# Optimization experiments

Measured on AMD Instinct MI355X. Metric: run time of the kernel, lower is better.

Reference implementation:

```python
import jax, jax.numpy as jnp
import numpy as np

B, S, HID = 2, 2048, 4096
NH, NKV, HD = 32, 8, 128
MAX_POS = 4096
SCALE = HD ** -0.5


def _rope_tables():
    inv_freq = 1.0 / (10000.0 ** (np.arange(0, HD, 2, dtype=np.float32) / HD))
    t = np.arange(MAX_POS, dtype=np.float32)
    freqs = np.outer(t, inv_freq)              # [MAX_POS, HD/2]
    emb = np.concatenate([freqs, freqs], axis=-1)  # [MAX_POS, HD]
    return jnp.asarray(np.cos(emb)), jnp.asarray(np.sin(emb))


def setup_inputs() -> dict:
    key = jax.random.key(0)
    ks = jax.random.split(key, 6)
    hidden_states = jax.random.normal(ks[0], (B, S, HID), dtype=jnp.float32)
    position_ids = jnp.broadcast_to(jnp.arange(S, dtype=jnp.int64 if jax.config.jax_enable_x64 else jnp.int32), (B, S))
    cos_table, sin_table = _rope_tables()
    # weights stored [in, out] for x @ W
    sd = HID ** -0.5
    Wq = jax.random.normal(ks[1], (HID, NH * HD), dtype=jnp.float32) * sd
    Wk = jax.random.normal(ks[2], (HID, NKV * HD), dtype=jnp.float32) * sd
    Wv = jax.random.normal(ks[3], (HID, NKV * HD), dtype=jnp.float32) * sd
    Wo = jax.random.normal(ks[4], (NH * HD, HID), dtype=jnp.float32) * sd
    return {"hidden_states": hidden_states, "position_ids": position_ids,
            "cos_table": cos_table, "sin_table": sin_table,
            "Wq": Wq, "Wk": Wk, "Wv": Wv, "Wo": Wo}


def _rotate_half(x):
    x1, x2 = jnp.split(x, 2, axis=-1)
    return jnp.concatenate([-x2, x1], axis=-1)


def reference(hidden_states, position_ids, cos_table, sin_table, Wq, Wk, Wv, Wo):
    b, s, _ = hidden_states.shape
    q = (hidden_states @ Wq).reshape(b, s, NH, HD)
    k = (hidden_states @ Wk).reshape(b, s, NKV, HD)
    v = (hidden_states @ Wv).reshape(b, s, NKV, HD)

    # RoPE, cos/sin gathered by position and unsqueezed at head dim (dim=2, bsnd)
    cos = cos_table[position_ids][:, :, None, :]  # [b, s, 1, hd]
    sin = sin_table[position_ids][:, :, None, :]
    q = q * cos + _rotate_half(q) * sin
    k = k * cos + _rotate_half(k) * sin

    # GQA: expand kv heads to match query heads
    rep = NH // NKV
    k = jnp.repeat(k, rep, axis=2)  # [b, s, NH, hd]
    v = jnp.repeat(v, rep, axis=2)

    scores = jnp.einsum('bqnd,bknd->bnqk', q, k) * SCALE  # [b, NH, s, s]
    causal = jnp.tril(jnp.ones((s, s), dtype=bool))
    scores = jnp.where(causal, scores, jnp.finfo(scores.dtype).min)
    probs = jax.nn.softmax(scores, axis=-1)
    attn = jnp.einsum('bnqk,bknd->bqnd', probs, v)  # [b, s, NH, hd]
    attn = attn.reshape(b, s, NH * HD)
    return attn @ Wo
```

## Files before the change

### kernel.cpp

```cpp
#include <hip/hip_runtime.h>
#include <stdint.h>

typedef unsigned short u16;
typedef __bf16 bf16x8 __attribute__((ext_vector_type(8)));
typedef unsigned short u16x8 __attribute__((ext_vector_type(8)));
typedef unsigned short u16x4 __attribute__((ext_vector_type(4)));
typedef float f32x4 __attribute__((ext_vector_type(4)));

#define B_ 2
#define S_ 2048
#define HID_ 4096
#define NH_ 32
#define NKV_ 8
#define HD_ 128
#define NTOT_ 6144
#define SCALE_ 0.08838834764831845f

#define GLD16(gp, lp)                                                     \
  __builtin_amdgcn_global_load_lds(                                       \
      (__attribute__((address_space(1))) void*)(gp),                      \
      (__attribute__((address_space(3))) void*)(lp), 16, 0, 0)

__device__ __forceinline__ u16 f2b(float f) {
  union { float f; uint32_t u; } v; v.f = f;
  uint32_t u = v.u;
  u = u + 0x7fffu + ((u >> 16) & 1u);
  return (u16)(u >> 16);
}
__device__ __forceinline__ float b2f(u16 s) {
  union { uint32_t u; float f; } v; v.u = ((uint32_t)s) << 16;
  return v.f;
}
__device__ __forceinline__ bf16x8 ldb8(const u16* p) {
  u16x8 u = *(const u16x8*)p;
  return __builtin_bit_cast(bf16x8, u);
}
__device__ __forceinline__ bf16x8 ldb8b(const char* p) {
  u16x8 u = *(const u16x8*)p;
  return __builtin_bit_cast(bf16x8, u);
}

__global__ __launch_bounds__(256) void k_convx(const float* __restrict__ src,
                                               u16* __restrict__ dst, int n4) {
  int i = blockIdx.x * 256 + threadIdx.x;
  if (i >= n4) return;
  const float4 v = ((const float4*)src)[i];
  u16x4 o = { f2b(v.x), f2b(v.y), f2b(v.z), f2b(v.w) };
  *(u16x4*)(dst + (size_t)i * 4) = o;
}

__global__ __launch_bounds__(256) void k_convT(const float* __restrict__ src,
                                               u16* __restrict__ dst, int N, int Kd) {
  __shared__ u16 tile[64][65];
  int k0 = blockIdx.x * 64, n0 = blockIdx.y * 64;
  int t = threadIdx.x;
  int rr = t >> 4;
  int cc = (t & 15) * 4;
#pragma unroll
  for (int p = 0; p < 4; ++p) {
    int r = p * 16 + rr;
    float4 v = *(const float4*)&src[(size_t)(k0 + r) * N + n0 + cc];
    tile[cc + 0][r] = f2b(v.x);
    tile[cc + 1][r] = f2b(v.y);
    tile[cc + 2][r] = f2b(v.z);
    tile[cc + 3][r] = f2b(v.w);
  }
  __syncthreads();
#pragma unroll
  for (int p = 0; p < 4; ++p) {
    int n = p * 16 + rr;
    u16x4 o = { tile[n][cc], tile[n][cc + 1], tile[n][cc + 2], tile[n][cc + 3] };
    *(u16x4*)&dst[(size_t)(n0 + n) * Kd + k0 + cc] = o;
  }
}

template <int MODE>
__device__ __forceinline__ void gemm_body(const u16* __restrict__ A,
                                          const u16* __restrict__ Bt,
                                          float* __restrict__ Cf,
                                          u16* __restrict__ Qb,
                                          u16* __restrict__ Kb,
                                          u16* __restrict__ Vb,
                                          int M, int N, int Kd) {
  __shared__ __align__(16) char smem[131072];
  const int NT = Kd >> 6;

  int nwg = gridDim.x * gridDim.y;
  int orig = blockIdx.y * gridDim.x + blockIdx.x;
  int cpx = nwg >> 3;
  int swz = (orig & 7) * cpx + (orig >> 3);
  int bx = swz % gridDim.x, by = swz / gridDim.x;
  int m0 = by * 256, n0 = bx * 256;

  int t = threadIdx.x, lane = t & 63, wave = t >> 6;
  int wr = wave >> 2, wc = wave & 3;
  int lg = lane >> 4, l16 = lane & 15;
  int loff = l16 * 64 + ((lg ^ ((l16 >> 1) & 3)) << 4);
  int srow = lane >> 2, schk = (lane & 3) ^ ((lane >> 3) & 3);

  const u16* Asrc = A  + (size_t)(m0 + wave * 32 + srow) * Kd + schk * 8;
  const u16* Bsrc = Bt + (size_t)(n0 + wave * 32 + srow) * Kd + schk * 8;

  f32x4 acc[8][4] = {};

#define STG_A(kt, kc) do {                                                          \
    char* d_ = smem + (((kt) & 1) << 16) + ((kc) << 14) + (wave << 11);             \
    const u16* s_ = Asrc + (size_t)(kt) * 64 + (kc) * 32;                           \
    GLD16(s_, d_); GLD16(s_ + (size_t)16 * Kd, d_ + 1024); } while (0)
#define STG_B(kt, kc) do {                                                          \
    char* d_ = smem + (((kt) & 1) << 16) + 32768 + ((kc) << 14) + (wave << 11);     \
    const u16* s_ = Bsrc + (size_t)(kt) * 64 + (kc) * 32;                           \
    GLD16(s_, d_); GLD16(s_ + (size_t)16 * Kd, d_ + 1024); } while (0)

  STG_A(0, 0); STG_B(0, 0); STG_A(0, 1); STG_B(0, 1);
  asm volatile("s_waitcnt vmcnt(0)" ::: "memory");
  __syncthreads();

  for (int kt = 0; kt < NT; ++kt) {
    const char* bufA = smem + ((kt & 1) << 16);
    const char* bufB = bufA + 32768;
    bool pf = (kt + 1 < NT);
    bf16x8 bfr[4], af[4];

#pragma unroll
    for (int j = 0; j < 4; ++j) bfr[j] = ldb8b(bufB + ((wc * 4 + j) << 10) + loff);
#pragma unroll
    for (int i = 0; i < 4; ++i) af[i] = ldb8b(bufA + ((wr * 8 + i) << 10) + loff);
    if (pf) STG_A(kt + 1, 0);
    __builtin_amdgcn_s_barrier();
    __builtin_amdgcn_s_setprio(1);
#pragma unroll
    for (int i = 0; i < 4; ++i)
#pragma unroll
      for (int j = 0; j < 4; ++j)
        acc[i][j] = __builtin_amdgcn_mfma_f32_16x16x32_bf16(af[i], bfr[j], acc[i][j], 0, 0, 0);
    __builtin_amdgcn_s_setprio(0);
    __builtin_amdgcn_s_barrier();

#pragma unroll
    for (int i = 0; i < 4; ++i) af[i] = ldb8b(bufA + ((wr * 8 + 4 + i) << 10) + loff);
    if (pf) STG_B(kt + 1, 0);
    __builtin_amdgcn_s_barrier();
    __builtin_amdgcn_s_setprio(1);
#pragma unroll
    for (int i = 0; i < 4; ++i)
#pragma unroll
      for (int j = 0; j < 4; ++j)
        acc[4 + i][j] = __builtin_amdgcn_mfma_f32_16x16x32_bf16(af[i], bfr[j], acc[4 + i][j], 0, 0, 0);
    __builtin_amdgcn_s_setprio(0);
    asm volatile("s_waitcnt vmcnt(4)" ::: "memory");
    __builtin_amdgcn_s_barrier();

#pragma unroll
    for (int j = 0; j < 4; ++j) bfr[j] = ldb8b(bufB + 16384 + ((wc * 4 + j) << 10) + loff);
#pragma unroll
    for (int i = 0; i < 4; ++i) af[i] = ldb8b(bufA + 16384 + ((wr * 8 + i) << 10) + loff);
    if (pf) STG_A(kt + 1, 1);
    __builtin_amdgcn_s_barrier();
    __builtin_amdgcn_s_setprio(1);
#pragma unroll
    for (int i = 0; i < 4; ++i)
#pragma unroll
      for (int j = 0; j < 4; ++j)
        acc[i][j] = __builtin_amdgcn_mfma_f32_16x16x32_bf16(af[i], bfr[j], acc[i][j], 0, 0, 0);
    __builtin_amdgcn_s_setprio(0);
    __builtin_amdgcn_s_barrier();

#pragma unroll
    for (int i = 0; i < 4; ++i) af[i] = ldb8b(bufA + 16384 + ((wr * 8 + 4 + i) << 10) + loff);
    if (pf) STG_B(kt + 1, 1);
    __builtin_amdgcn_s_barrier();
    __builtin_amdgcn_s_setprio(1);
#pragma unroll
    for (int i = 0; i < 4; ++i)
#pragma unroll
      for (int j = 0; j < 4; ++j)
        acc[4 + i][j] = __builtin_amdgcn_mfma_f32_16x16x32_bf16(af[i], bfr[j], acc[4 + i][j], 0, 0, 0);
    __builtin_amdgcn_s_setprio(0);
    asm volatile("s_waitcnt vmcnt(4)" ::: "memory");
    __builtin_amdgcn_s_barrier();
  }
#undef STG_A
#undef STG_B

  if (MODE == 1) {
#pragma unroll
    for (int i = 0; i < 8; ++i)
#pragma unroll
      for (int j = 0; j < 4; ++j)
#pragma unroll
        for (int r = 0; r < 4; ++r) {
          int m = m0 + wr * 128 + i * 16 + lg * 4 + r;
          int n = n0 + wc * 64 + j * 16 + l16;
          Cf[(size_t)m * N + n] = acc[i][j][r];
        }
  } else {
    int slice = (n0 >> 7) + (wc >> 1);
#pragma unroll
    for (int i = 0; i < 8; ++i)
#pragma unroll
      for (int j = 0; j < 4; ++j)
#pragma unroll
        for (int r = 0; r < 4; ++r) {
          int m = m0 + wr * 128 + i * 16 + lg * 4 + r;
          int d = ((wc & 1) << 6) + j * 16 + l16;
          int b = m >> 11, s = m & (S_ - 1);
          u16 val = f2b(acc[i][j][r]);
          if (slice < NH_) {
            Qb[(((size_t)b * NH_ + slice) * S_ + s) * HD_ + d] = val;
          } else if (slice < NH_ + NKV_) {
            Kb[(((size_t)b * NKV_ + (slice - NH_)) * S_ + s) * HD_ + d] = val;
          } else {
            Vb[(((size_t)b * NKV_ + (slice - NH_ - NKV_)) * HD_ + d) * S_ + s] = val;
          }
        }
  }
}

__global__ __launch_bounds__(512, 2) void k_gemm_qkv(const u16* __restrict__ A,
                                                     const u16* __restrict__ Bt,
                                                     u16* __restrict__ Qb,
                                                     u16* __restrict__ Kb,
                                                     u16* __restrict__ Vb,
                                                     int M, int N, int Kd) {
  gemm_body<0>(A, Bt, nullptr, Qb, Kb, Vb, M, N, Kd);
}

__global__ __launch_bounds__(512, 2) void k_gemm_out(const u16* __restrict__ A,
                                                     const u16* __restrict__ Bt,
                                                     float* __restrict__ Cf,
                                                     int M, int N, int Kd) {
  gemm_body<1>(A, Bt, Cf, nullptr, nullptr, nullptr, M, N, Kd);
}

__global__ __launch_bounds__(256) void k_rope(u16* __restrict__ buf, const int* __restrict__ pos,
                                              const float* __restrict__ ct, const float* __restrict__ st,
                                              int H, int rows) {
  int wave = threadIdx.x >> 6, lane = threadIdx.x & 63;
  int row = blockIdx.x * 4 + wave;
  if (row >= rows) return;
  int s = row & (S_ - 1);
  int b = row / (H * S_);
  int p = pos[b * S_ + s];
  size_t base = (size_t)row * HD_;
  float x1 = b2f(buf[base + lane]);
  float x2 = b2f(buf[base + 64 + lane]);
  float c  = ct[(size_t)p * HD_ + lane];
  float sn = st[(size_t)p * HD_ + lane];
  buf[base + lane]      = f2b(x1 * c - x2 * sn);
  buf[base + 64 + lane] = f2b(x2 * c + x1 * sn);
}

__global__ __launch_bounds__(256, 4) void k_attn(const u16* __restrict__ Q,
                                                 const u16* __restrict__ K,
                                                 const u16* __restrict__ Vt,
                                                 u16* __restrict__ Ob) {
  __shared__ __align__(16) char smem[40960];
  const int VS_OFF = 16384, PS_OFF = 32768;

  int bid = blockIdx.x;
  int pid = bid & 15;
  int h   = (bid >> 4) & 31;
  int b   = bid >> 9;
  int kvh = h >> 2;
  int tid = threadIdx.x;
  int wave = tid >> 6, lane = tid & 63;
  int lg = lane >> 4, l16 = lane & 15;
  int lsw = (l16 & 7) << 4;

  const u16* Qp = Q  + (((size_t)b * NH_  + h)   * S_) * HD_;
  const u16* Kp = K  + (((size_t)b * NKV_ + kvh) * S_) * HD_;
  const u16* Vp = Vt + (((size_t)b * NKV_ + kvh) * HD_) * S_;

  for (int pass = 0; pass < 2; ++pass) {
    int qt = pass ? (31 - pid) : pid;
    int q0 = qt * 64 + wave * 16;
    int qg = q0 + l16;

    bf16x8 qf[4];
#pragma unroll
    for (int c = 0; c < 4; ++c)
      qf[c] = ldb8(&Qp[(size_t)qg * HD_ + c * 32 + lg * 8]);

    f32x4 oacc[8] = {};
    float mrun = -1e30f, lrun = 0.f;

    int nt = qt + 1;
    for (int tI = 0; tI < nt; ++tI) {
      int kb = tI * 64;
      __syncthreads();
#pragma unroll
      for (int i = 0; i < 4; ++i) {
        int ci = i * 256 + tid;
        int r = ci >> 4, ch = ci & 15;
        u16x8 v = *(const u16x8*)&Kp[(size_t)(kb + r) * HD_ + ch * 8];
        *(u16x8*)(smem + r * 256 + ((ch * 16) ^ ((r & 7) << 4))) = v;
      }
#pragma unroll
      for (int i = 0; i < 4; ++i) {
        int ci = i * 256 + tid;
        int r = ci >> 3, ch = ci & 7;
        u16x8 v = *(const u16x8*)&Vp[(size_t)r * S_ + kb + ch * 8];
        *(u16x8*)(smem + VS_OFF + r * 128 + ((ch * 16) ^ ((r & 7) << 4))) = v;
      }
      __syncthreads();

      f32x4 sc[4] = {};
#pragma unroll
      for (int c = 0; c < 4; ++c) {
#pragma unroll
        for (int n = 0; n < 4; ++n) {
          bf16x8 kf = ldb8b(smem + (n * 16 + l16) * 256 + ((c * 64 + lg * 16) ^ lsw));
          sc[n] = __builtin_amdgcn_mfma_f32_16x16x32_bf16(kf, qf[c], sc[n], 0, 0, 0);
        }
      }

      bool diag = (tI == qt);
      float mx = -1e30f;
#pragma unroll
      for (int n = 0; n < 4; ++n)
#pragma unroll
        for (int r = 0; r < 4; ++r) {
          float v = sc[n][r];
          int key = kb + n * 16 + lg * 4 + r;
          if (diag && key > qg) v = -1e30f;
          sc[n][r] = v;
          mx = fmaxf(mx, v);
        }
      mx = fmaxf(mx, __shfl_xor(mx, 16));
      mx = fmaxf(mx, __shfl_xor(mx, 32));
      float mnew = fmaxf(mrun, mx * SCALE_);
      float alpha = __expf(mrun - mnew);
      float ps = 0.f;
#pragma unroll
      for (int n = 0; n < 4; ++n) {
        u16x4 pk;
#pragma unroll
        for (int r = 0; r < 4; ++r) {
          float p = __expf(fmaf(sc[n][r], SCALE_, -mnew));
          ps += p;
          pk[r] = f2b(p);
        }
        *(u16x4*)(smem + PS_OFF + wave * 2048 + l16 * 128 + ((n * 32 + lg * 8) ^ lsw)) = pk;
      }
      ps += __shfl_xor(ps, 16);
      ps += __shfl_xor(ps, 32);
      lrun = lrun * alpha + ps;
      mrun = mnew;

      float ar[4];
#pragma unroll
      for (int r = 0; r < 4; ++r) ar[r] = __shfl(alpha, lg * 4 + r);
#pragma unroll
      for (int ns = 0; ns < 8; ++ns)
#pragma unroll
        for (int r = 0; r < 4; ++r) oacc[ns][r] *= ar[r];

#pragma unroll
      for (int ck = 0; ck < 2; ++ck) {
        bf16x8 pa = ldb8b(smem + PS_OFF + wave * 2048 + l16 * 128 + ((ck * 64 + lg * 16) ^ lsw));
#pragma unroll
        for (int ns = 0; ns < 8; ++ns) {
          bf16x8 vf = ldb8b(smem + VS_OFF + (ns * 16 + l16) * 128 + ((ck * 64 + lg * 16) ^ lsw));
          oacc[ns] = __builtin_amdgcn_mfma_f32_16x16x32_bf16(pa, vf, oacc[ns], 0, 0, 0);
        }
      }
    }

    float lr[4];
#pragma unroll
    for (int r = 0; r < 4; ++r) lr[r] = 1.0f / __shfl(lrun, lg * 4 + r);
#pragma unroll
    for (int ns = 0; ns < 8; ++ns)
#pragma unroll
      for (int r = 0; r < 4; ++r) {
        int q = q0 + lg * 4 + r;
        Ob[((size_t)(b * S_) + q) * (NH_ * HD_) + h * HD_ + ns * 16 + l16] =
            f2b(oacc[ns][r] * lr[r]);
      }
  }
}

extern "C" void kernel_launch(void* const* d_in, const int* in_sizes, int n_in,
                              void* d_out, int out_size, void* d_ws, size_t ws_size,
                              hipStream_t stream) {
  const float* hs  = (const float*)d_in[0];
  const int*   pos = (const int*)d_in[1];
  const float* ct  = (const float*)d_in[2];
  const float* st  = (const float*)d_in[3];
  const float* Wq  = (const float*)d_in[4];
  const float* Wk  = (const float*)d_in[5];
  const float* Wv  = (const float*)d_in[6];
  const float* Wo  = (const float*)d_in[7];
  float* out = (float*)d_out;

  char* w = (char*)d_ws;
  u16* Xb    = (u16*)(w);
  u16* WqkvT = (u16*)(w + 33554432ull);
  u16* WoT   = (u16*)(w + 83886080ull);
  u16* Qb    = (u16*)(w + 117440512ull);
  u16* Kb    = (u16*)(w + 150994944ull);
  u16* Vb    = (u16*)(w + 159383552ull);
  u16* Attb  = (u16*)(w + 167772160ull);

  k_convx<<<16384, 256, 0, stream>>>(hs, Xb, 4194304);
  k_convT<<<dim3(64, 64), 256, 0, stream>>>(Wq, WqkvT, 4096, 4096);
  k_convT<<<dim3(64, 16), 256, 0, stream>>>(Wk, WqkvT + (size_t)4096 * 4096, 1024, 4096);
  k_convT<<<dim3(64, 16), 256, 0, stream>>>(Wv, WqkvT + (size_t)5120 * 4096, 1024, 4096);
  k_convT<<<dim3(64, 64), 256, 0, stream>>>(Wo, WoT, 4096, 4096);
  k_gemm_qkv<<<dim3(24, 16), 512, 0, stream>>>(Xb, WqkvT, Qb, Kb, Vb, 4096, NTOT_, 4096);
  k_rope<<<32768, 256, 0, stream>>>(Qb, pos, ct, st, NH_, B_ * NH_ * S_);
  k_rope<<<8192, 256, 0, stream>>>(Kb, pos, ct, st, NKV_, B_ * NKV_ * S_);
  k_attn<<<1024, 256, 0, stream>>>(Qb, Kb, Vb, Attb);
  k_gemm_out<<<dim3(16, 16), 512, 0, stream>>>(Attb, WoT, out, 4096, 4096, 4096);
}
```

Measured before the change: 636.8 us.

## Retile QKV GEMM to 256x192 tiles for 512 workgroups

Replaces the shared templated GEMM for the QKV projection with a dedicated kernel using 256x192 output tiles, giving a 32x16 grid of 512 workgroups instead of 24x16=384, which should fill the 256 CUs in two even waves. LDS layout and B staging are reworked for the 3-column fragment layout, and the epilogue computes head per column. Also drops the (512,2) occupancy hint and adds a full vmcnt drain on the last iteration. The narrower tile lowers MFMA work per LDS load and so reduces arithmetic intensity per workgroup.

```diff
diff --git a/kernel.cpp b/kernel.cpp
--- a/kernel.cpp
+++ b/kernel.cpp
@@ -74,14 +74,10 @@
   }
 }
 
-template <int MODE>
-__device__ __forceinline__ void gemm_body(const u16* __restrict__ A,
-                                          const u16* __restrict__ Bt,
-                                          float* __restrict__ Cf,
-                                          u16* __restrict__ Qb,
-                                          u16* __restrict__ Kb,
-                                          u16* __restrict__ Vb,
-                                          int M, int N, int Kd) {
+__global__ __launch_bounds__(512) void k_gemm_out(const u16* __restrict__ A,
+                                                  const u16* __restrict__ Bt,
+                                                  float* __restrict__ Cf,
+                                                  int M, int N, int Kd) {
   __shared__ __align__(16) char smem[131072];
   const int NT = Kd >> 6;
 
@@ -148,7 +144,8 @@
       for (int j = 0; j < 4; ++j)
         acc[4 + i][j] = __builtin_amdgcn_mfma_f32_16x16x32_bf16(af[i], bfr[j], acc[4 + i][j], 0, 0, 0);
     __builtin_amdgcn_s_setprio(0);
-    asm volatile("s_waitcnt vmcnt(4)" ::: "memory");
+    if (pf) { asm volatile("s_waitcnt vmcnt(4)" ::: "memory"); }
+    else    { asm volatile("s_waitcnt vmcnt(0)" ::: "memory"); }
     __builtin_amdgcn_s_barrier();
 
 #pragma unroll
@@ -177,60 +174,155 @@
       for (int j = 0; j < 4; ++j)
         acc[4 + i][j] = __builtin_amdgcn_mfma_f32_16x16x32_bf16(af[i], bfr[j], acc[4 + i][j], 0, 0, 0);
     __builtin_amdgcn_s_setprio(0);
-    asm volatile("s_waitcnt vmcnt(4)" ::: "memory");
+    if (pf) { asm volatile("s_waitcnt vmcnt(4)" ::: "memory"); }
     __builtin_amdgcn_s_barrier();
   }
 #undef STG_A
 #undef STG_B
 
-  if (MODE == 1) {
-#pragma unroll
-    for (int i = 0; i < 8; ++i)
-#pragma unroll
-      for (int j = 0; j < 4; ++j)
-#pragma unroll
-        for (int r = 0; r < 4; ++r) {
-          int m = m0 + wr * 128 + i * 16 + lg * 4 + r;
-          int n = n0 + wc * 64 + j * 16 + l16;
-          Cf[(size_t)m * N + n] = acc[i][j][r];
+#pragma unroll
+  for (int i = 0; i < 8; ++i)
+#pragma unroll
+    for (int j = 0; j < 4; ++j)
+#pragma unroll
+      for (int r = 0; r < 4; ++r) {
+        int m = m0 + wr * 128 + i * 16 + lg * 4 + r;
+        int n = n0 + wc * 64 + j * 16 + l16;
+        Cf[(size_t)m * N + n] = acc[i][j][r];
+      }
+}
+
+__global__ __launch_bounds__(512) void k_gqkv(const u16* __restrict__ A,
+                                              const u16* __restrict__ Bt,
+                                              u16* __restrict__ Qb,
+                                              u16* __restrict__ Kb,
+                                              u16* __restrict__ Vb) {
+  __shared__ __align__(16) char smem[114688];
+  const int Kd = HID_;
+  const int NT = Kd >> 6;
+
+  int orig = blockIdx.y * 32 + blockIdx.x;
+  int swz = (orig & 7) * 64 + (orig >> 3);
+  int bx = swz & 31, by = swz >> 5;
+  int m0 = by * 256, n0 = bx * 192;
+
+  int t = threadIdx.x, lane = t & 63, wave = t >> 6;
+  int wr = wave >> 2, wc = wave & 3;
+  int lg = lane >> 4, l16 = lane & 15;
+  int loff = l16 * 64 + ((lg ^ ((l16 >> 1) & 3)) << 4);
+  int srow = lane >> 2, schk = (lane & 3) ^ ((lane >> 3) & 3);
+
+  const u16* sA0 = A + (size_t)(m0 + wave * 32 + srow) * Kd + schk * 8;
+  const u16* sB0 = Bt + (size_t)(n0 + wave * 16 + srow) * Kd + schk * 8;
+  const u16* sB1 = Bt + (size_t)(n0 + 128 + (wave & 3) * 16 + srow) * Kd + schk * 8;
+  int bdst2 = (8 + (wave & 3)) << 10;
+
+  f32x4 acc[8][3] = {};
+
+#define QAOFF(kt, kc) ((((kt) & 1) * 57344) + ((kc) << 14))
+#define QBOFF(kt, kc) ((((kt) & 1) * 57344) + 32768 + (kc) * 12288)
+#define STG_A(kt, kc) do {                                                          \
+    char* d_ = smem + QAOFF(kt, kc) + (wave << 11);                                 \
+    const u16* s_ = sA0 + (size_t)(kt) * 64 + (kc) * 32;                            \
+    GLD16(s_, d_); GLD16(s_ + (size_t)16 * Kd, d_ + 1024); } while (0)
+#define STG_B(kt, kc) do {                                                          \
+    char* db_ = smem + QBOFF(kt, kc);                                               \
+    GLD16(sB0 + (size_t)(kt) * 64 + (kc) * 32, db_ + (wave << 10));                 \
+    GLD16(sB1 + (size_t)(kt) * 64 + (kc) * 32, db_ + bdst2); } while (0)
+
+  STG_A(0, 0); STG_B(0, 0); STG_A(0, 1); STG_B(0, 1);
+  asm volatile("s_waitcnt vmcnt(0)" ::: "memory");
+  __syncthreads();
+
+  for (int kt = 0; kt < NT; ++kt) {
+    const char* bufA = smem + ((kt & 1) * 57344);
+    const char* bufB = bufA + 32768;
+    bool pf = (kt + 1 < NT);
+    bf16x8 bfr[3], af[4];
+
+#pragma unroll
+    for (int j = 0; j < 3; ++j) bfr[j] = ldb8b(bufB + ((wc * 3 + j) << 10) + loff);
+#pragma unroll
+    for (int i = 0; i < 4; ++i) af[i] = ldb8b(bufA + ((wr * 8 + i) << 10) + loff);
+    if (pf) STG_A(kt + 1, 0);
+    __builtin_amdgcn_s_barrier();
+    __builtin_amdgcn_s_setprio(1);
+#pragma unroll
+    for (int i = 0; i < 4; ++i)
+#pragma unroll
+      for (int j = 0; j < 3; ++j)
+        acc[i][j] = __builtin_amdgcn_mfma_f32_16x16x32_bf16(af[i], bfr[j], acc[i][j], 0, 0, 0);
+    __builtin_amdgcn_s_setprio(0);
+    __builtin_amdgcn_s_barrier();
+
+#pragma unroll
+    for (int i = 0; i < 4; ++i) af[i] = ldb8b(bufA + ((wr * 8 + 4 + i) << 10) + loff);
+    if (pf) STG_B(kt + 1, 0);
+    __builtin_amdgcn_s_barrier();
+    __builtin_amdgcn_s_setprio(1);
+#pragma unroll
+    for (int i = 0; i < 4; ++i)
+#pragma unroll
+      for (int j = 0; j < 3; ++j)
+        acc[4 + i][j] = __builtin_amdgcn_mfma_f32_16x16x32_bf16(af[i], bfr[j], acc[4 + i][j], 0, 0, 0);
+    __builtin_amdgcn_s_setprio(0);
+    if (pf) { asm volatile("s_waitcnt vmcnt(4)" ::: "memory"); }
+    else    { asm volatile("s_waitcnt vmcnt(0)" ::: "memory"); }
+    __builtin_amdgcn_s_barrier();
+
+#pragma unroll
+    for (int j = 0; j < 3; ++j) bfr[j] = ldb8b(bufB + 12288 + ((wc * 3 + j) << 10) + loff);
+#pragma unroll
+    for (int i = 0; i < 4; ++i) af[i] = ldb8b(bufA + 16384 + ((wr * 8 + i) << 10) + loff);
+    if (pf) STG_A(kt + 1, 1);
+    __builtin_amdgcn_s_barrier();
+    __builtin_amdgcn_s_setprio(1);
+#pragma unroll
+    for (int i = 0; i < 4; ++i)
+#pragma unroll
+      for (int j = 0; j < 3; ++j)
+        acc[i][j] = __builtin_amdgcn_mfma_f32_16x16x32_bf16(af[i], bfr[j], acc[i][j], 0, 0, 0);
+    __builtin_amdgcn_s_setprio(0);
+    __builtin_amdgcn_s_barrier();
+
+#pragma unroll
+    for (int i = 0; i < 4; ++i) af[i] = ldb8b(bufA + 16384 + ((wr * 8 + 4 + i) << 10) + loff);
+    if (pf) STG_B(kt + 1, 1);
+    __builtin_amdgcn_s_barrier();
+    __builtin_amdgcn_s_setprio(1);
+#pragma unroll
+    for (int i = 0; i < 4; ++i)
+#pragma unroll
+      for (int j = 0; j < 3; ++j)
+        acc[4 + i][j] = __builtin_amdgcn_mfma_f32_16x16x32_bf16(af[i], bfr[j], acc[4 + i][j], 0, 0, 0);
+    __builtin_amdgcn_s_setprio(0);
+    if (pf) { asm volatile("s_waitcnt vmcnt(4)" ::: "memory"); }
+    __builtin_amdgcn_s_barrier();
+  }
+#undef STG_A
+#undef STG_B
+#undef QAOFF
+#undef QBOFF
+
+#pragma unroll
+  for (int i = 0; i < 8; ++i)
+#pragma unroll
+    for (int j = 0; j < 3; ++j)
+#pragma unroll
+      for (int r = 0; r < 4; ++r) {
+        int m = m0 + wr * 128 + i * 16 + lg * 4 + r;
+        int n = n0 + wc * 48 + j * 16 + l16;
+        int head = n >> 7, d = n & 127;
+        int b = m >> 11, s = m & (S_ - 1);
+        u16 val = f2b(acc[i][j][r]);
+        if (head < NH_) {
+          Qb[(((size_t)b * NH_ + head) * S_ + s) * HD_ + d] = val;
+        } else if (head < NH_ + NKV_) {
+          Kb[(((size_t)b * NKV_ + (head - NH_)) * S_ + s) * HD_ + d] = val;
+        } else {
+          Vb[(((size_t)b * NKV_ + (head - NH_ - NKV_)) * HD_ + d) * S_ + s] = val;
         }
-  } else {
-    int slice = (n0 >> 7) + (wc >> 1);
-#pragma unroll
-    for (int i = 0; i < 8; ++i)
-#pragma unroll
-      for (int j = 0; j < 4; ++j)
-#pragma unroll
-        for (int r = 0; r < 4; ++r) {
-          int m = m0 + wr * 128 + i * 16 + lg * 4 + r;
-          int d = ((wc & 1) << 6) + j * 16 + l16;
-          int b = m >> 11, s = m & (S_ - 1);
-          u16 val = f2b(acc[i][j][r]);
-          if (slice < NH_) {
-            Qb[(((size_t)b * NH_ + slice) * S_ + s) * HD_ + d] = val;
-          } else if (slice < NH_ + NKV_) {
-            Kb[(((size_t)b * NKV_ + (slice - NH_)) * S_ + s) * HD_ + d] = val;
-          } else {
-            Vb[(((size_t)b * NKV_ + (slice - NH_ - NKV_)) * HD_ + d) * S_ + s] = val;
-          }
-        }
-  }
-}
-
-__global__ __launch_bounds__(512, 2) void k_gemm_qkv(const u16* __restrict__ A,
-                                                     const u16* __restrict__ Bt,
-                                                     u16* __restrict__ Qb,
-                                                     u16* __restrict__ Kb,
-                                                     u16* __restrict__ Vb,
-                                                     int M, int N, int Kd) {
-  gemm_body<0>(A, Bt, nullptr, Qb, Kb, Vb, M, N, Kd);
-}
-
-__global__ __launch_bounds__(512, 2) void k_gemm_out(const u16* __restrict__ A,
-                                                     const u16* __restrict__ Bt,
-                                                     float* __restrict__ Cf,
-                                                     int M, int N, int Kd) {
-  gemm_body<1>(A, Bt, Cf, nullptr, nullptr, nullptr, M, N, Kd);
+      }
 }
 
 __global__ __launch_bounds__(256) void k_rope(u16* __restrict__ buf, const int* __restrict__ pos,
@@ -408,7 +500,7 @@
   k_convT<<<dim3(64, 16), 256, 0, stream>>>(Wk, WqkvT + (size_t)4096 * 4096, 1024, 4096);
   k_convT<<<dim3(64, 16), 256, 0, stream>>>(Wv, WqkvT + (size_t)5120 * 4096, 1024, 4096);
   k_convT<<<dim3(64, 64), 256, 0, stream>>>(Wo, WoT, 4096, 4096);
-  k_gemm_qkv<<<dim3(24, 16), 512, 0, stream>>>(Xb, WqkvT, Qb, Kb, Vb, 4096, NTOT_, 4096);
+  k_gqkv<<<dim3(32, 16), 512, 0, stream>>>(Xb, WqkvT, Qb, Kb, Vb);
   k_rope<<<32768, 256, 0, stream>>>(Qb, pos, ct, st, NH_, B_ * NH_ * S_);
   k_rope<<<8192, 256, 0, stream>>>(Kb, pos, ct, st, NKV_, B_ * NKV_ * S_);
   k_attn<<<1024, 256, 0, stream>>>(Qb, Kb, Vb, Attb);
```

New measurement: 624.6 us. About the same (-1.9%).
